# Performance work log

Hardware: AMD Instinct MI355X
Metric: run time of the kernel (lower is better)

Reference implementation:

```python
import jax, jax.numpy as jnp
import numpy as np

EPS = 1e-6
N_HEADS = 16
D_HEAD = 64

def _rmsnorm(x, scale):
    rms = jnp.sqrt(jnp.mean(x * x, axis=-1, keepdims=True) + EPS)
    return x / rms * scale

def setup_inputs() -> dict:
    key = jax.random.key(0)
    ks = jax.random.split(key, 8)
    B, L, D = 512, 64, 1024
    return {
        "x": jax.random.normal(ks[0], (B, L, D), dtype=jnp.float32),
        "rel_indices": jax.random.randint(ks[1], (L, L), 0, 225, dtype=jnp.int64),
        "Wq": jax.random.normal(ks[2], (D, D), dtype=jnp.float32) * 0.02,
        "Wk": jax.random.normal(ks[3], (D, D), dtype=jnp.float32) * 0.02,
        "Wv": jax.random.normal(ks[4], (D, D), dtype=jnp.float32) * 0.02,
        "Wo": jax.random.normal(ks[5], (D, D), dtype=jnp.float32) * 0.02,
        "q_scale": jnp.ones((D_HEAD,), dtype=jnp.float32),
        "k_scale": jnp.ones((D_HEAD,), dtype=jnp.float32),
        "rel_k": jax.random.normal(ks[6], (225, D_HEAD), dtype=jnp.float32) * 0.02,
        "rel_v": jax.random.normal(ks[7], (225, D_HEAD), dtype=jnp.float32) * 0.02,
    }

def reference(x, rel_indices, Wq, Wk, Wv, Wo, q_scale, k_scale, rel_k, rel_v):
    B, L, D = x.shape
    H, dk = N_HEADS, D_HEAD
    scale = 1.0 / jnp.sqrt(jnp.float32(dk))
    # projections; Linear with weight W applied as x @ W (bias=False)
    q = (x @ Wq).reshape(B, L, H, dk)
    k = (x @ Wk).reshape(B, L, H, dk)
    v = (x @ Wv).reshape(B, L, H, dk).transpose(0, 2, 1, 3)  # bhld
    q = _rmsnorm(q, q_scale).transpose(0, 2, 1, 3)  # bhld
    k = _rmsnorm(k, k_scale).transpose(0, 2, 1, 3)  # bhld
    r_k = rel_k[rel_indices]  # [L, L, dk]
    r_v = rel_v[rel_indices]  # [L, L, dk]
    content = jnp.einsum('bhid,bhjd->bhij', q, k)
    rel = jnp.einsum('bhid,ijd->bhij', q, r_k)
    probs = jax.nn.softmax((content + rel) * scale, axis=-1)
    out = jnp.einsum('bhij,bhjd->bhid', probs, v) + jnp.einsum('bhij,ijd->bhid', probs, r_v)
    out = out.transpose(0, 2, 1, 3).reshape(B, L, D)
    return out @ Wo
```

## Files before the change

### kernel.cpp

```cpp
#include <hip/hip_runtime.h>
#include <stdint.h>

typedef unsigned short u16;
typedef __attribute__((ext_vector_type(8))) short s16x8;
typedef __attribute__((ext_vector_type(4))) float f32x4;

#define DEV static __device__ __forceinline__

#define MFMA16(a, b, c) __builtin_amdgcn_mfma_f32_16x16x32_bf16((a), (b), (c), 0, 0, 0)

DEV u16 f2b(float f) {
  unsigned u = __float_as_uint(f);
  unsigned r = (u + 0x7fffu + ((u >> 16) & 1u)) >> 16;
  return (u16)r;
}

typedef const __attribute__((address_space(1))) unsigned int* as1p;
typedef __attribute__((address_space(3))) unsigned int* as3p;

DEV void gload16(const void* g, void* l) {
  __builtin_amdgcn_global_load_lds((as1p)(uintptr_t)g, (as3p)(unsigned)(uintptr_t)l, 16, 0, 0);
}

__global__ void conv_x_k(const float* __restrict__ x, u16* __restrict__ xb) {
  const int n8 = 32768 * 1024 / 8;
  int i = blockIdx.x * 256 + threadIdx.x;
  int stride = gridDim.x * 256;
  for (; i < n8; i += stride) {
    const float4* p = (const float4*)x + (size_t)i * 2;
    float4 a = p[0], c = p[1];
    union { s16x8 v; u16 u[8]; } o;
    o.u[0] = f2b(a.x); o.u[1] = f2b(a.y); o.u[2] = f2b(a.z); o.u[3] = f2b(a.w);
    o.u[4] = f2b(c.x); o.u[5] = f2b(c.y); o.u[6] = f2b(c.z); o.u[7] = f2b(c.w);
    *(s16x8*)(xb + (size_t)i * 8) = o.v;
  }
}

__global__ void transp_w_k(const float* __restrict__ Wq, const float* __restrict__ Wk,
                           const float* __restrict__ Wv, const float* __restrict__ Wo,
                           u16* __restrict__ wqkT, u16* __restrict__ wvT, u16* __restrict__ woT) {
  const int z = blockIdx.z;
  const float* src = z == 0 ? Wq : z == 1 ? Wk : z == 2 ? Wv : Wo;
  u16* dst = z == 0 ? wqkT : z == 1 ? (wqkT + 1024 * 1024) : z == 2 ? wvT : woT;
  __shared__ u16 t[64][72];
  const int kb = blockIdx.y * 64, nb = blockIdx.x * 64;
  const int tid = threadIdx.x;
  const int c = tid & 63, r0 = tid >> 6;
  #pragma unroll
  for (int s = 0; s < 16; ++s) {
    int r = r0 * 16 + s;
    t[r][c] = f2b(src[(size_t)(kb + r) * 1024 + nb + c]);
  }
  __syncthreads();
  #pragma unroll
  for (int s = 0; s < 16; ++s) {
    int n = r0 * 16 + s;
    dst[(size_t)(nb + n) * 1024 + kb + c] = t[c][n];
  }
}

__global__ void prep_rel_k(const float* __restrict__ rk, const float* __restrict__ rv,
                           u16* __restrict__ rkb, u16* __restrict__ rvT) {
  int i = blockIdx.x * 256 + threadIdx.x;
  if (i < 240 * 64) {
    int tt = i >> 6, d = i & 63;
    rkb[i] = (tt < 225) ? f2b(rk[tt * 64 + d]) : (u16)0;
  }
  if (i < 64 * 256) {
    int d = i >> 8, tt = i & 255;
    rvT[i] = (tt < 225) ? f2b(rv[tt * 64 + d]) : (u16)0;
  }
}

template <int EPI>
__global__ __launch_bounds__(256, 2)
void gemm_k(const u16* __restrict__ A, const u16* __restrict__ BT,
            u16* __restrict__ o16a, u16* __restrict__ o16b,
            float* __restrict__ oF,
            const float* __restrict__ qsc, const float* __restrict__ ksc) {
  __shared__ u16 smA[2][128 * 32];
  __shared__ u16 smB[2][128 * 32];
  const int tid = threadIdx.x;
  const int w = tid >> 6, l = tid & 63;
  const int lc = l & 15, l4 = l >> 4;
  const int m0 = blockIdx.y * 128, n0 = blockIdx.x * 128;
  const int wm = (w >> 1) * 64, wn = (w & 1) * 64;

  f32x4 acc[4][4];
  #pragma unroll
  for (int i = 0; i < 4; ++i)
    #pragma unroll
    for (int j = 0; j < 4; ++j) acc[i][j] = (f32x4){0.f, 0.f, 0.f, 0.f};

  int srcRow[2], srcCol[2];
  #pragma unroll
  for (int s = 0; s < 2; ++s) {
    int p = w * 2048 + s * 1024 + l * 16;
    int row = p >> 6;
    int lb = p ^ (((row ^ (row >> 2)) & 3) << 4);
    srcRow[s] = row;
    srcCol[s] = (lb & 63) >> 1;
  }

  auto stage = [&](int buf, int kt) {
    #pragma unroll
    for (int s = 0; s < 2; ++s) {
      int base = w * 2048 + s * 1024;
      const u16* ga = A + (size_t)(m0 + srcRow[s]) * 1024 + kt * 32 + srcCol[s];
      gload16(ga, (char*)&smA[buf][0] + base);
      const u16* gb = BT + (size_t)(n0 + srcRow[s]) * 1024 + kt * 32 + srcCol[s];
      gload16(gb, (char*)&smB[buf][0] + base);
    }
  };
  auto fragA = [&](int buf, int mf) -> s16x8 {
    int row = wm + mf * 16 + lc;
    int p = (row << 6) + (l4 << 4);
    p ^= ((row ^ (row >> 2)) & 3) << 4;
    return *(const s16x8*)((const char*)&smA[buf][0] + p);
  };
  auto fragB = [&](int buf, int nf) -> s16x8 {
    int row = wn + nf * 16 + lc;
    int p = (row << 6) + (l4 << 4);
    p ^= ((row ^ (row >> 2)) & 3) << 4;
    return *(const s16x8*)((const char*)&smB[buf][0] + p);
  };

  stage(0, 0);
  __syncthreads();
  #pragma unroll 2
  for (int kt = 0; kt < 32; ++kt) {
    int cur = kt & 1;
    if (kt + 1 < 32) stage(cur ^ 1, kt + 1);
    s16x8 af[4], bf[4];
    #pragma unroll
    for (int i = 0; i < 4; ++i) { af[i] = fragA(cur, i); bf[i] = fragB(cur, i); }
    #pragma unroll
    for (int mf = 0; mf < 4; ++mf)
      #pragma unroll
      for (int nf = 0; nf < 4; ++nf)
        acc[mf][nf] = MFMA16(af[mf], bf[nf], acc[mf][nf]);
    __syncthreads();
  }

  if constexpr (EPI == 2) {
    #pragma unroll
    for (int mf = 0; mf < 4; ++mf)
      #pragma unroll
      for (int r = 0; r < 4; ++r) {
        int gm = m0 + wm + mf * 16 + l4 * 4 + r;
        #pragma unroll
        for (int nf = 0; nf < 4; ++nf) {
          int gn = n0 + wn + nf * 16 + lc;
          oF[(size_t)gm * 1024 + gn] = acc[mf][nf][r];
        }
      }
  } else if constexpr (EPI == 1) {
    #pragma unroll
    for (int mf = 0; mf < 4; ++mf)
      #pragma unroll
      for (int r = 0; r < 4; ++r) {
        int gm = m0 + wm + mf * 16 + l4 * 4 + r;
        #pragma unroll
        for (int nf = 0; nf < 4; ++nf) {
          int gn = n0 + wn + nf * 16 + lc;
          size_t addr = (((size_t)(gn >> 6) * 16 + (gm >> 6)) * 64 + (gm & 63)) * 64 + (gn & 63);
          o16a[addr] = f2b(acc[mf][nf][r]);
        }
      }
  } else {
    int nw0 = n0 + wn;
    bool isq = nw0 < 1024;
    const float* sc = isq ? qsc : ksc;
    u16* dst = isq ? o16a : o16b;
    int h = (nw0 & 1023) >> 6;
    float scv[4];
    #pragma unroll
    for (int nf = 0; nf < 4; ++nf) scv[nf] = sc[nf * 16 + lc];
    #pragma unroll
    for (int mf = 0; mf < 4; ++mf)
      #pragma unroll
      for (int r = 0; r < 4; ++r) {
        float ss = 0.f;
        #pragma unroll
        for (int nf = 0; nf < 4; ++nf) ss += acc[mf][nf][r] * acc[mf][nf][r];
        #pragma unroll
        for (int mask = 1; mask < 16; mask <<= 1) ss += __shfl_xor(ss, mask, 64);
        float rinv = rsqrtf(ss * 0.015625f + 1e-6f);
        int gm = m0 + wm + mf * 16 + l4 * 4 + r;
        size_t base = (((size_t)(gm >> 6) * 16 + h) * 64 + (gm & 63)) * 64;
        #pragma unroll
        for (int nf = 0; nf < 4; ++nf)
          dst[base + nf * 16 + lc] = f2b(acc[mf][nf][r] * rinv * scv[nf]);
      }
  }
}

DEV int rwIdx(int row, int col) {
  int c16 = (col >> 2) ^ (row & 7);
  return row * 256 + (c16 << 2) + (col & 3);
}

__global__ __launch_bounds__(256, 2)
void attn_k(const u16* __restrict__ qn, const u16* __restrict__ kn,
            const u16* __restrict__ vT, const u16* __restrict__ rkb,
            const u16* __restrict__ rvT, const int* __restrict__ ridx,
            u16* __restrict__ ao) {
  __shared__ float Rw[64 * 256];
  __shared__ u16 Pl[64 * 72];
  const int bid = blockIdx.x;
  const int b = bid >> 4, h = bid & 15;
  const int tid = threadIdx.x;
  const int w = tid >> 6, l = tid & 63;
  const int lc = l & 15, l4 = l >> 4;
  const int i0 = w * 16;
  const size_t hb = (size_t)(b * 16 + h) * 4096;
  const u16* qh = qn + hb;
  const u16* kh = kn + hb;
  const u16* vh = vT + hb;

  s16x8 aq0 = *(const s16x8*)(qh + (i0 + lc) * 64 + l4 * 8);
  s16x8 aq1 = *(const s16x8*)(qh + (i0 + lc) * 64 + 32 + l4 * 8);
  f32x4 accC[4];
  #pragma unroll
  for (int nf = 0; nf < 4; ++nf) accC[nf] = (f32x4){0.f, 0.f, 0.f, 0.f};
  #pragma unroll
  for (int nf = 0; nf < 4; ++nf) {
    s16x8 b0 = *(const s16x8*)(kh + (nf * 16 + lc) * 64 + l4 * 8);
    s16x8 b1 = *(const s16x8*)(kh + (nf * 16 + lc) * 64 + 32 + l4 * 8);
    accC[nf] = MFMA16(aq0, b0, accC[nf]);
    accC[nf] = MFMA16(aq1, b1, accC[nf]);
  }
  #pragma unroll
  for (int nf = 0; nf < 15; ++nf) {
    f32x4 rr = (f32x4){0.f, 0.f, 0.f, 0.f};
    s16x8 b0 = *(const s16x8*)(rkb + (nf * 16 + lc) * 64 + l4 * 8);
    s16x8 b1 = *(const s16x8*)(rkb + (nf * 16 + lc) * 64 + 32 + l4 * 8);
    rr = MFMA16(aq0, b0, rr);
    rr = MFMA16(aq1, b1, rr);
    int t = nf * 16 + lc;
    #pragma unroll
    for (int q = 0; q < 4; ++q) Rw[rwIdx(i0 + l4 * 4 + q, t)] = rr[q];
  }
  __syncthreads();
  float ev[4][4];
  int ts[4][4];
  float linv[4];
  #pragma unroll
  for (int q = 0; q < 4; ++q) {
    int row = i0 + l4 * 4 + q;
    float mx = -1e30f;
    #pragma unroll
    for (int nf = 0; nf < 4; ++nf) {
      int j = nf * 16 + lc;
      int t = ridx[row * 64 + j];
      ts[nf][q] = t;
      float s = (accC[nf][q] + Rw[rwIdx(row, t)]) * 0.125f;
      ev[nf][q] = s;
      mx = fmaxf(mx, s);
    }
    #pragma unroll
    for (int mask = 1; mask < 16; mask <<= 1) mx = fmaxf(mx, __shfl_xor(mx, mask, 64));
    float sum = 0.f;
    #pragma unroll
    for (int nf = 0; nf < 4; ++nf) { float e = __expf(ev[nf][q] - mx); ev[nf][q] = e; sum += e; }
    #pragma unroll
    for (int mask = 1; mask < 16; mask <<= 1) sum += __shfl_xor(sum, mask, 64);
    linv[q] = 1.f / sum;
    #pragma unroll
    for (int nf = 0; nf < 4; ++nf) Pl[row * 72 + nf * 16 + lc] = f2b(ev[nf][q]);
  }
  __syncthreads();
  {
    f32x4 z = (f32x4){0.f, 0.f, 0.f, 0.f};
    for (int c = tid; c < 64 * 256 / 4; c += 256) ((f32x4*)Rw)[c] = z;
  }
  __syncthreads();
  #pragma unroll
  for (int q = 0; q < 4; ++q)
    #pragma unroll
    for (int nf = 0; nf < 4; ++nf)
      atomicAdd(&Rw[rwIdx(i0 + l4 * 4 + q, ts[nf][q])], ev[nf][q]);
  __syncthreads();
  f32x4 accO[4];
  #pragma unroll
  for (int nf = 0; nf < 4; ++nf) accO[nf] = (f32x4){0.f, 0.f, 0.f, 0.f};
  s16x8 pa0 = *(const s16x8*)(&Pl[(i0 + lc) * 72 + l4 * 8]);
  s16x8 pa1 = *(const s16x8*)(&Pl[(i0 + lc) * 72 + 32 + l4 * 8]);
  #pragma unroll
  for (int nf = 0; nf < 4; ++nf) {
    s16x8 b0 = *(const s16x8*)(vh + (nf * 16 + lc) * 64 + l4 * 8);
    s16x8 b1 = *(const s16x8*)(vh + (nf * 16 + lc) * 64 + 32 + l4 * 8);
    accO[nf] = MFMA16(pa0, b0, accO[nf]);
    accO[nf] = MFMA16(pa1, b1, accO[nf]);
  }
  #pragma unroll
  for (int ks = 0; ks < 8; ++ks) {
    int row = i0 + lc;
    int c16 = ks * 8 + l4 * 2;
    f32x4 w0 = *(const f32x4*)&Rw[row * 256 + ((c16 ^ (row & 7)) << 2)];
    f32x4 w1 = *(const f32x4*)&Rw[row * 256 + (((c16 + 1) ^ (row & 7)) << 2)];
    union { s16x8 v; u16 u[8]; } wa;
    #pragma unroll
    for (int j = 0; j < 4; ++j) { wa.u[j] = f2b(w0[j]); wa.u[4 + j] = f2b(w1[j]); }
    #pragma unroll
    for (int nf = 0; nf < 4; ++nf) {
      s16x8 rb = *(const s16x8*)(rvT + (nf * 16 + lc) * 256 + ks * 32 + l4 * 8);
      accO[nf] = MFMA16(wa.v, rb, accO[nf]);
    }
  }
  #pragma unroll
  for (int q = 0; q < 4; ++q) {
    int row = i0 + l4 * 4 + q;
    #pragma unroll
    for (int nf = 0; nf < 4; ++nf) {
      int d = nf * 16 + lc;
      ao[((size_t)(b * 64 + row)) * 1024 + h * 64 + d] = f2b(accO[nf][q] * linv[q]);
    }
  }
}

extern "C" void kernel_launch(void* const* d_in, const int* in_sizes, int n_in,
                              void* d_out, int out_size, void* d_ws, size_t ws_size,
                              hipStream_t stream) {
  (void)in_sizes; (void)n_in; (void)out_size; (void)ws_size;
  const float* x  = (const float*)d_in[0];
  const int* ridx = (const int*)d_in[1];
  const float* Wq = (const float*)d_in[2];
  const float* Wk = (const float*)d_in[3];
  const float* Wv = (const float*)d_in[4];
  const float* Wo = (const float*)d_in[5];
  const float* qs = (const float*)d_in[6];
  const float* ks = (const float*)d_in[7];
  const float* rk = (const float*)d_in[8];
  const float* rv = (const float*)d_in[9];
  float* out = (float*)d_out;

  char* ws = (char*)d_ws;
  const size_t SZ = 32768ull * 1024 * 2;
  u16* xb   = (u16*)(ws);
  u16* qn   = (u16*)(ws + SZ);
  u16* kn   = (u16*)(ws + 2 * SZ);
  u16* vT   = (u16*)(ws + 3 * SZ);
  u16* wqkT = (u16*)(ws + 4 * SZ);
  u16* wvT  = (u16*)(ws + 4 * SZ + 4194304);
  u16* woT  = (u16*)(ws + 4 * SZ + 6291456);
  u16* rkb  = (u16*)(ws + 4 * SZ + 8388608);
  u16* rvTb = (u16*)(ws + 4 * SZ + 8388608 + 30720);

  conv_x_k<<<2048, 256, 0, stream>>>(x, xb);
  transp_w_k<<<dim3(16, 16, 4), 256, 0, stream>>>(Wq, Wk, Wv, Wo, wqkT, wvT, woT);
  prep_rel_k<<<64, 256, 0, stream>>>(rk, rv, rkb, rvTb);
  gemm_k<0><<<dim3(16, 256), 256, 0, stream>>>(xb, wqkT, qn, kn, nullptr, qs, ks);
  gemm_k<1><<<dim3(256, 8), 256, 0, stream>>>(wvT, xb, vT, nullptr, nullptr, nullptr, nullptr);
  attn_k<<<8192, 256, 0, stream>>>(qn, kn, vT, rkb, rvTb, ridx, xb);
  gemm_k<2><<<dim3(8, 256), 256, 0, stream>>>(xb, woT, nullptr, nullptr, out, nullptr, nullptr);
}
```

Measured before the change: 1.039 ms.

## Store relative-weight buffer as bf16 with packed LDS atomics and remap GEMM tiles

The attention kernel's relative-position scratch buffer moves from fp32 to bf16. This halves its LDS footprint and allows three workgroups per CU. The fp32 atomicAdd scatter is replaced by ds_pk_add_bf16, so the probabilities are accumulated in bf16, which costs some precision. K, V and index loads are hoisted and batched, and the GEMM kernel gets a workgroup remap intended to improve L2 locality.

```diff
diff --git a/kernel.cpp b/kernel.cpp
--- a/kernel.cpp
+++ b/kernel.cpp
@@ -14,12 +14,18 @@
   unsigned r = (u + 0x7fffu + ((u >> 16) & 1u)) >> 16;
   return (u16)r;
 }
+DEV float b2f(u16 u) { return __uint_as_float(((unsigned)u) << 16); }
 
 typedef const __attribute__((address_space(1))) unsigned int* as1p;
 typedef __attribute__((address_space(3))) unsigned int* as3p;
 
 DEV void gload16(const void* g, void* l) {
   __builtin_amdgcn_global_load_lds((as1p)(uintptr_t)g, (as3p)(unsigned)(uintptr_t)l, 16, 0, 0);
+}
+
+DEV void ldsPkAddBf16(void* ldsPtr, unsigned packed) {
+  unsigned addr = (unsigned)(uintptr_t)ldsPtr;
+  asm volatile("ds_pk_add_bf16 %0, %1" : : "v"(addr), "v"(packed) : "memory");
 }
 
 __global__ void conv_x_k(const float* __restrict__ x, u16* __restrict__ xb) {
@@ -83,7 +89,11 @@
   const int tid = threadIdx.x;
   const int w = tid >> 6, l = tid & 63;
   const int lc = l & 15, l4 = l >> 4;
-  const int m0 = blockIdx.y * 128, n0 = blockIdx.x * 128;
+  const int nwg = gridDim.x * gridDim.y;
+  const int orig = blockIdx.y * gridDim.x + blockIdx.x;
+  const int wg = ((orig & 7) * (nwg >> 3)) + (orig >> 3);
+  const int bx = wg % gridDim.x, by = wg / gridDim.x;
+  const int m0 = by * 128, n0 = bx * 128;
   const int wm = (w >> 1) * 64, wn = (w & 1) * 64;
 
   f32x4 acc[4][4];
@@ -195,17 +205,16 @@
   }
 }
 
-DEV int rwIdx(int row, int col) {
-  int c16 = (col >> 2) ^ (row & 7);
-  return row * 256 + (c16 << 2) + (col & 3);
-}
-
-__global__ __launch_bounds__(256, 2)
+DEV int rwByte(int row, int t) {
+  return row * 512 + ((((t >> 3) ^ (row & 7)) << 4)) + ((t & 7) * 2);
+}
+
+__global__ __launch_bounds__(256, 3)
 void attn_k(const u16* __restrict__ qn, const u16* __restrict__ kn,
             const u16* __restrict__ vT, const u16* __restrict__ rkb,
             const u16* __restrict__ rvT, const int* __restrict__ ridx,
             u16* __restrict__ ao) {
-  __shared__ float Rw[64 * 256];
+  __shared__ u16 RW[64 * 256];
   __shared__ u16 Pl[64 * 72];
   const int bid = blockIdx.x;
   const int b = bid >> 4, h = bid & 15;
@@ -218,32 +227,58 @@
   const u16* kh = kn + hb;
   const u16* vh = vT + hb;
 
+  int ts[4][4];
+  #pragma unroll
+  for (int q = 0; q < 4; ++q) {
+    int row = i0 + l4 * 4 + q;
+    #pragma unroll
+    for (int nf = 0; nf < 4; ++nf) ts[nf][q] = ridx[row * 64 + nf * 16 + lc];
+  }
   s16x8 aq0 = *(const s16x8*)(qh + (i0 + lc) * 64 + l4 * 8);
   s16x8 aq1 = *(const s16x8*)(qh + (i0 + lc) * 64 + 32 + l4 * 8);
+  s16x8 kb0[4], kb1[4], vb0[4], vb1[4];
+  #pragma unroll
+  for (int nf = 0; nf < 4; ++nf) {
+    kb0[nf] = *(const s16x8*)(kh + (nf * 16 + lc) * 64 + l4 * 8);
+    kb1[nf] = *(const s16x8*)(kh + (nf * 16 + lc) * 64 + 32 + l4 * 8);
+    vb0[nf] = *(const s16x8*)(vh + (nf * 16 + lc) * 64 + l4 * 8);
+    vb1[nf] = *(const s16x8*)(vh + (nf * 16 + lc) * 64 + 32 + l4 * 8);
+  }
+
   f32x4 accC[4];
   #pragma unroll
   for (int nf = 0; nf < 4; ++nf) accC[nf] = (f32x4){0.f, 0.f, 0.f, 0.f};
   #pragma unroll
   for (int nf = 0; nf < 4; ++nf) {
-    s16x8 b0 = *(const s16x8*)(kh + (nf * 16 + lc) * 64 + l4 * 8);
-    s16x8 b1 = *(const s16x8*)(kh + (nf * 16 + lc) * 64 + 32 + l4 * 8);
-    accC[nf] = MFMA16(aq0, b0, accC[nf]);
-    accC[nf] = MFMA16(aq1, b1, accC[nf]);
-  }
-  #pragma unroll
-  for (int nf = 0; nf < 15; ++nf) {
-    f32x4 rr = (f32x4){0.f, 0.f, 0.f, 0.f};
-    s16x8 b0 = *(const s16x8*)(rkb + (nf * 16 + lc) * 64 + l4 * 8);
-    s16x8 b1 = *(const s16x8*)(rkb + (nf * 16 + lc) * 64 + 32 + l4 * 8);
-    rr = MFMA16(aq0, b0, rr);
-    rr = MFMA16(aq1, b1, rr);
-    int t = nf * 16 + lc;
-    #pragma unroll
-    for (int q = 0; q < 4; ++q) Rw[rwIdx(i0 + l4 * 4 + q, t)] = rr[q];
-  }
-  __syncthreads();
+    accC[nf] = MFMA16(aq0, kb0[nf], accC[nf]);
+    accC[nf] = MFMA16(aq1, kb1[nf], accC[nf]);
+  }
+
+  #pragma unroll
+  for (int c = 0; c < 3; ++c) {
+    s16x8 rb0[5], rb1[5];
+    #pragma unroll
+    for (int u = 0; u < 5; ++u) {
+      int t0 = (c * 5 + u) * 16;
+      rb0[u] = *(const s16x8*)(rkb + (t0 + lc) * 64 + l4 * 8);
+      rb1[u] = *(const s16x8*)(rkb + (t0 + lc) * 64 + 32 + l4 * 8);
+    }
+    #pragma unroll
+    for (int u = 0; u < 5; ++u) {
+      f32x4 rr = (f32x4){0.f, 0.f, 0.f, 0.f};
+      rr = MFMA16(aq0, rb0[u], rr);
+      rr = MFMA16(aq1, rb1[u], rr);
+      int t = (c * 5 + u) * 16 + lc;
+      #pragma unroll
+      for (int q = 0; q < 4; ++q) {
+        int row = i0 + l4 * 4 + q;
+        RW[rwByte(row, t) >> 1] = f2b(rr[q]);
+      }
+    }
+  }
+  __syncthreads();
+
   float ev[4][4];
-  int ts[4][4];
   float linv[4];
   #pragma unroll
   for (int q = 0; q < 4; ++q) {
@@ -251,10 +286,8 @@
     float mx = -1e30f;
     #pragma unroll
     for (int nf = 0; nf < 4; ++nf) {
-      int j = nf * 16 + lc;
-      int t = ridx[row * 64 + j];
-      ts[nf][q] = t;
-      float s = (accC[nf][q] + Rw[rwIdx(row, t)]) * 0.125f;
+      float r = b2f(RW[rwByte(row, ts[nf][q]) >> 1]);
+      float s = (accC[nf][q] + r) * 0.125f;
       ev[nf][q] = s;
       mx = fmaxf(mx, s);
     }
@@ -270,44 +303,58 @@
     for (int nf = 0; nf < 4; ++nf) Pl[row * 72 + nf * 16 + lc] = f2b(ev[nf][q]);
   }
   __syncthreads();
-  {
-    f32x4 z = (f32x4){0.f, 0.f, 0.f, 0.f};
-    for (int c = tid; c < 64 * 256 / 4; c += 256) ((f32x4*)Rw)[c] = z;
-  }
-  __syncthreads();
-  #pragma unroll
-  for (int q = 0; q < 4; ++q)
-    #pragma unroll
-    for (int nf = 0; nf < 4; ++nf)
-      atomicAdd(&Rw[rwIdx(i0 + l4 * 4 + q, ts[nf][q])], ev[nf][q]);
-  __syncthreads();
+
   f32x4 accO[4];
   #pragma unroll
   for (int nf = 0; nf < 4; ++nf) accO[nf] = (f32x4){0.f, 0.f, 0.f, 0.f};
   s16x8 pa0 = *(const s16x8*)(&Pl[(i0 + lc) * 72 + l4 * 8]);
   s16x8 pa1 = *(const s16x8*)(&Pl[(i0 + lc) * 72 + 32 + l4 * 8]);
+  {
+    s16x8 z;
+    #pragma unroll
+    for (int j = 0; j < 8; ++j) z[j] = 0;
+    #pragma unroll
+    for (int zz = 0; zz < 8; ++zz) ((s16x8*)RW)[zz * 256 + tid] = z;
+  }
   #pragma unroll
   for (int nf = 0; nf < 4; ++nf) {
-    s16x8 b0 = *(const s16x8*)(vh + (nf * 16 + lc) * 64 + l4 * 8);
-    s16x8 b1 = *(const s16x8*)(vh + (nf * 16 + lc) * 64 + 32 + l4 * 8);
-    accO[nf] = MFMA16(pa0, b0, accO[nf]);
-    accO[nf] = MFMA16(pa1, b1, accO[nf]);
-  }
-  #pragma unroll
-  for (int ks = 0; ks < 8; ++ks) {
-    int row = i0 + lc;
-    int c16 = ks * 8 + l4 * 2;
-    f32x4 w0 = *(const f32x4*)&Rw[row * 256 + ((c16 ^ (row & 7)) << 2)];
-    f32x4 w1 = *(const f32x4*)&Rw[row * 256 + (((c16 + 1) ^ (row & 7)) << 2)];
-    union { s16x8 v; u16 u[8]; } wa;
-    #pragma unroll
-    for (int j = 0; j < 4; ++j) { wa.u[j] = f2b(w0[j]); wa.u[4 + j] = f2b(w1[j]); }
+    accO[nf] = MFMA16(pa0, vb0[nf], accO[nf]);
+    accO[nf] = MFMA16(pa1, vb1[nf], accO[nf]);
+  }
+  __syncthreads();
+
+  #pragma unroll
+  for (int q = 0; q < 4; ++q)
     #pragma unroll
     for (int nf = 0; nf < 4; ++nf) {
-      s16x8 rb = *(const s16x8*)(rvT + (nf * 16 + lc) * 256 + ks * 32 + l4 * 8);
-      accO[nf] = MFMA16(wa.v, rb, accO[nf]);
-    }
-  }
+      int row = i0 + l4 * 4 + q;
+      int t = ts[nf][q];
+      int byte = row * 512 + ((((t >> 3) ^ (row & 7)) << 4)) + ((t & 6) * 2);
+      unsigned pk = ((unsigned)f2b(ev[nf][q])) << ((t & 1) * 16);
+      ldsPkAddBf16((char*)RW + byte, pk);
+    }
+  asm volatile("s_waitcnt lgkmcnt(0)" ::: "memory");
+  __syncthreads();
+
+  #pragma unroll
+  for (int kc = 0; kc < 4; ++kc) {
+    s16x8 rb[2][4], wa[2];
+    #pragma unroll
+    for (int s = 0; s < 2; ++s) {
+      int ks = kc * 2 + s;
+      int row = i0 + lc;
+      wa[s] = *(const s16x8*)((const char*)RW + row * 512 + ((((ks * 4 + l4) ^ (row & 7))) << 4));
+      #pragma unroll
+      for (int nf = 0; nf < 4; ++nf)
+        rb[s][nf] = *(const s16x8*)(rvT + (nf * 16 + lc) * 256 + ks * 32 + l4 * 8);
+    }
+    #pragma unroll
+    for (int s = 0; s < 2; ++s)
+      #pragma unroll
+      for (int nf = 0; nf < 4; ++nf)
+        accO[nf] = MFMA16(wa[s], rb[s][nf], accO[nf]);
+  }
+
   #pragma unroll
   for (int q = 0; q < 4; ++q) {
     int row = i0 + l4 * 4 + q;
```

Measured after the change: 966.0 us. 7.0% less time.
